# Optimization experiments

Measured on AMD Instinct MI355X. Metric: run time of the kernel, lower is better.

Reference implementation:

```python
import jax, jax.numpy as jnp
import numpy as np

B, L, E, H = 1024, 50, 256, 256
NEG = -1e9          # stands in for -inf masked_fill (exp(NEG) == 0 in fp32)
C_EXPL = 10.0       # tanh_exploration for the pointer head
N_GLIMPSES = 1


def setup_inputs() -> dict:
    key = jax.random.key(0)
    ks = jax.random.split(key, 20)
    s = 1.0 / np.sqrt(H).astype(np.float32)
    return {
        "decoder_input": jax.random.normal(ks[0], (B, E), jnp.float32),
        "embedded_inputs": jax.random.normal(ks[1], (L, B, E), jnp.float32),
        "h0": jax.random.normal(ks[2], (B, H), jnp.float32),
        "c0": jax.random.normal(ks[3], (B, H), jnp.float32),
        "context": jax.random.normal(ks[4], (L, B, H), jnp.float32),
        "init_mask": jnp.zeros((B, L), dtype=bool),
        "lstm_Wih": jax.random.normal(ks[5], (4 * H, E), jnp.float32) * s,
        "lstm_Whh": jax.random.normal(ks[6], (4 * H, H), jnp.float32) * s,
        "lstm_bih": jax.random.normal(ks[7], (4 * H,), jnp.float32) * s,
        "lstm_bhh": jax.random.normal(ks[8], (4 * H,), jnp.float32) * s,
        "gl_Wq": jax.random.normal(ks[9], (H, H), jnp.float32) * s,
        "gl_bq": jax.random.normal(ks[10], (H,), jnp.float32) * s,
        "gl_Wref": jax.random.normal(ks[11], (H, H), jnp.float32) * s,
        "gl_bref": jax.random.normal(ks[12], (H,), jnp.float32) * s,
        "gl_v": jax.random.uniform(ks[13], (H,), jnp.float32, -s, s),
        "pt_Wq": jax.random.normal(ks[14], (H, H), jnp.float32) * s,
        "pt_bq": jax.random.normal(ks[15], (H, H // H * H,)[:1] and (H,), jnp.float32) * s,
        "pt_Wref": jax.random.normal(ks[16], (H, H), jnp.float32) * s,
        "pt_bref": jax.random.normal(ks[17], (H,), jnp.float32) * s,
        "pt_v": jax.random.uniform(ks[18], (H,), jnp.float32, -s, s),
    }


def _attention(Wq, bq, Wref, bref, v, query, context, use_tanh):
    # context: [L,B,H], query: [B,H]
    e = jnp.einsum('lbh,oh->lbo', context, Wref) + bref      # conv1d(k=1) proj of ref
    q = query @ Wq.T + bq                                    # [B,H]
    u = jnp.einsum('lbh,h->bl', jnp.tanh(q[None, :, :] + e), v)
    if use_tanh:
        u = C_EXPL * jnp.tanh(u)
    return e, u


def _lstm_cell(x, h, c, Wih, Whh, bih, bhh):
    g = x @ Wih.T + bih + h @ Whh.T + bhh
    i, f, gg, o = jnp.split(g, 4, axis=1)   # torch LSTMCell gate order: i,f,g,o
    c2 = jax.nn.sigmoid(f) * c + jax.nn.sigmoid(i) * jnp.tanh(gg)
    h2 = jax.nn.sigmoid(o) * jnp.tanh(c2)
    return h2, c2


def reference(decoder_input, embedded_inputs, h0, c0, context, init_mask,
              lstm_Wih, lstm_Whh, lstm_bih, lstm_bhh,
              gl_Wq, gl_bq, gl_Wref, gl_bref, gl_v,
              pt_Wq, pt_bq, pt_Wref, pt_bref, pt_v):
    batch_idx = jnp.arange(B)

    def step(carry, t):
        h, c, mask, idxs, dec_in = carry
        # update_mask(mask, selected), skipped at step 0 (prev_idxs is None)
        safe = jnp.maximum(idxs, 0)
        m2 = mask.at[batch_idx, safe].set(True)
        m2 = m2.at[:, -1].set(jnp.where(m2.all(axis=1), False, m2[:, -1]))
        logit_mask = jnp.where(t == 0, mask, m2)
        # LSTM cell
        hy, cy = _lstm_cell(dec_in, h, c, lstm_Wih, lstm_Whh, lstm_bih, lstm_bhh)
        g_l = hy
        # glimpse attention(s) (mask_glimpses=True)
        for _ in range(N_GLIMPSES):
            e, gl = _attention(gl_Wq, gl_bq, gl_Wref, gl_bref, gl_v, g_l, context, False)
            gl = jnp.where(logit_mask, NEG, gl)
            g_l = jnp.einsum('lbh,bl->bh', e, jax.nn.softmax(gl, axis=1))
        # pointer attention (mask_logits=True)
        _, logits = _attention(pt_Wq, pt_bq, pt_Wref, pt_bref, pt_v, g_l, context, True)
        logits = jnp.where(logit_mask, NEG, logits)
        log_p = jax.nn.log_softmax(logits, axis=1)          # [B,L]
        new_idxs = jax.lax.stop_gradient(jnp.argmax(log_p, axis=1))  # greedy decode (detached)
        new_dec_in = embedded_inputs[new_idxs, batch_idx]   # gather next input [B,E]
        return (hy, cy, logit_mask, new_idxs, new_dec_in), (log_p, new_idxs)

    init = (h0, c0, init_mask, jnp.full((B,), -1, dtype=jnp.int32), decoder_input)
    _, (log_ps, sels) = jax.lax.scan(step, init, jnp.arange(L))
    # stack along time dim 1, as torch.stack(outputs, 1)
    return jnp.transpose(log_ps, (1, 0, 2)), jnp.transpose(sels, (1, 0))
```

## Files before the change

kernel.cpp:

```cpp
#include <hip/hip_runtime.h>
#include <math.h>

#define Bsz 1024
#define Lsz 50
#define Esz 256
#define Hsz 256
#define NEGV (-1e9f)

__device__ __forceinline__ void gl_lds16(const float* g, float* l) {
#if __has_builtin(__builtin_amdgcn_global_load_lds)
    __builtin_amdgcn_global_load_lds(
        (const __attribute__((address_space(1))) unsigned int*)g,
        (__attribute__((address_space(3))) unsigned int*)l, 16, 0, 0);
#else
    *(float4*)l = *(const float4*)g;
#endif
}

__global__ __launch_bounds__(256) void eproj_pack(
    const float* __restrict__ A,
    const float* __restrict__ Wgl, const float* __restrict__ bgl, float* __restrict__ Egl,
    const float* __restrict__ Wpt, const float* __restrict__ bpt, float* __restrict__ Ept,
    const float* __restrict__ WqGl, const float* __restrict__ WqPt,
    float* __restrict__ WqGlP, float* __restrict__ WqPtP)
{
    __shared__ __align__(16) float As[16][68];
    __shared__ __align__(16) float Bs[16][68];
    const int tid = threadIdx.x;

    if (blockIdx.x >= 6400) {
        const int p = blockIdx.x - 6400;
        const int sel = p >> 8;
        const int k = p & 255;
        const float* src = sel ? WqPt : WqGl;
        float*       dst = sel ? WqPtP : WqGlP;
        dst[((size_t)(k >> 2) * 256 + tid) * 4 + (k & 3)] = src[(size_t)tid * 256 + k];
        return;
    }

    const int tx = tid & 15, ty = tid >> 4;
    const int ml = tid >> 2;
    const int kb = (tid & 3) << 2;

    const int x = blockIdx.x;
    const int xcd = x & 7;
    const int j = x >> 3;
    const int mt = xcd * 100 + (j >> 3);
    const int sel = (j >> 2) & 1;
    const int nt = j & 3;
    const float* W    = sel ? Wpt : Wgl;
    const float* bias = sel ? bpt : bgl;
    float*       Eo   = sel ? Ept : Egl;
    const int m0 = mt * 64, n0 = nt * 64;

    float4 a4 = *(const float4*)(A + (size_t)(m0 + ml) * 256 + kb);
    float4 b4 = *(const float4*)(W + (size_t)(n0 + ml) * 256 + kb);

    float acc[4][4] = {};
    for (int k0 = 0; k0 < 256; k0 += 16) {
        As[kb+0][ml] = a4.x; As[kb+1][ml] = a4.y; As[kb+2][ml] = a4.z; As[kb+3][ml] = a4.w;
        Bs[kb+0][ml] = b4.x; Bs[kb+1][ml] = b4.y; Bs[kb+2][ml] = b4.z; Bs[kb+3][ml] = b4.w;
        __syncthreads();
        int k1 = k0 + 16;
        if (k1 < 256) {
            a4 = *(const float4*)(A + (size_t)(m0 + ml) * 256 + k1 + kb);
            b4 = *(const float4*)(W + (size_t)(n0 + ml) * 256 + k1 + kb);
        }
#pragma unroll
        for (int kk = 0; kk < 16; kk++) {
            float4 av = *(const float4*)(&As[kk][ty << 2]);
            float4 bv = *(const float4*)(&Bs[kk][tx << 2]);
            float a_[4] = {av.x, av.y, av.z, av.w};
            float b_[4] = {bv.x, bv.y, bv.z, bv.w};
#pragma unroll
            for (int i = 0; i < 4; i++)
#pragma unroll
                for (int j2 = 0; j2 < 4; j2++) acc[i][j2] = fmaf(a_[i], b_[j2], acc[i][j2]);
        }
        __syncthreads();
    }
#pragma unroll
    for (int i = 0; i < 4; i++) {
        int m = m0 + (ty << 2) + i;
        int bb = m & (Bsz - 1);
        int ll = m >> 10;
#pragma unroll
        for (int j2 = 0; j2 < 4; j2++) {
            int n = n0 + (tx << 2) + j2;
            Eo[(size_t)bb * Lsz * Hsz + (size_t)ll * Hsz + n] = acc[i][j2] + bias[n];
        }
    }
}

__global__ __launch_bounds__(256) void lstm_fused(
    const float* __restrict__ dec, const float* __restrict__ hprev,
    const float* __restrict__ cin,
    const float* __restrict__ Wih, const float* __restrict__ Whh,
    const float* __restrict__ bih, const float* __restrict__ bhh,
    float* __restrict__ hout, float* __restrict__ cout)
{
    __shared__ __align__(16) float As[16][36];
    __shared__ __align__(16) float Bs[16][68];
    const int tid = threadIdx.x;
    const int tx = tid & 15, ty = tid >> 4;
    const int mlA = tid >> 3;
    const int kbA = (tid & 7) << 1;
    const int mlB = tid >> 2;
    const int kbB = (tid & 3) << 2;
    const int m0 = blockIdx.x * 32;
    const int hh0 = blockIdx.y * 16;
    const int wrow = ((mlB >> 4) << 8) + hh0 + (mlB & 15);
    const int pcol = ((mlB & 15) << 2) + (mlB >> 4);

    float2 a2 = *(const float2*)(dec + (size_t)(m0 + mlA) * 256 + kbA);
    float4 b4 = *(const float4*)(Wih + (size_t)wrow * 256 + kbB);

    float acc[2][4] = {};
    for (int k0 = 0; k0 < 512; k0 += 16) {
        As[kbA+0][mlA] = a2.x; As[kbA+1][mlA] = a2.y;
        Bs[kbB+0][pcol] = b4.x; Bs[kbB+1][pcol] = b4.y;
        Bs[kbB+2][pcol] = b4.z; Bs[kbB+3][pcol] = b4.w;
        __syncthreads();
        int k1 = k0 + 16;
        if (k1 < 512) {
            const float* Ap = (k1 < 256) ? dec : hprev;
            const float* Wp = (k1 < 256) ? Wih : Whh;
            int kk0 = k1 & 255;
            a2 = *(const float2*)(Ap + (size_t)(m0 + mlA) * 256 + kk0 + kbA);
            b4 = *(const float4*)(Wp + (size_t)wrow * 256 + kk0 + kbB);
        }
#pragma unroll
        for (int kk = 0; kk < 16; kk++) {
            float2 av = *(const float2*)(&As[kk][ty << 1]);
            float4 bv = *(const float4*)(&Bs[kk][tx << 2]);
            acc[0][0] = fmaf(av.x, bv.x, acc[0][0]);
            acc[0][1] = fmaf(av.x, bv.y, acc[0][1]);
            acc[0][2] = fmaf(av.x, bv.z, acc[0][2]);
            acc[0][3] = fmaf(av.x, bv.w, acc[0][3]);
            acc[1][0] = fmaf(av.y, bv.x, acc[1][0]);
            acc[1][1] = fmaf(av.y, bv.y, acc[1][1]);
            acc[1][2] = fmaf(av.y, bv.z, acc[1][2]);
            acc[1][3] = fmaf(av.y, bv.w, acc[1][3]);
        }
        __syncthreads();
    }

    const int hh = hh0 + tx;
    const float bi0 = bih[hh]       + bhh[hh];
    const float bf  = bih[256 + hh] + bhh[256 + hh];
    const float bg  = bih[512 + hh] + bhh[512 + hh];
    const float bo  = bih[768 + hh] + bhh[768 + hh];
#pragma unroll
    for (int i = 0; i < 2; i++) {
        int m = m0 + (ty << 1) + i;
        float gi = acc[i][0] + bi0;
        float gf = acc[i][1] + bf;
        float gc = acc[i][2] + bg;
        float go = acc[i][3] + bo;
        float ii = 1.0f / (1.0f + expf(-gi));
        float ff = 1.0f / (1.0f + expf(-gf));
        float oo = 1.0f / (1.0f + expf(-go));
        float c2 = ff * cin[(size_t)m * 256 + hh] + ii * tanhf(gc);
        hout[(size_t)m * 256 + hh] = oo * tanhf(c2);
        cout[(size_t)m * 256 + hh] = c2;
    }
}

__global__ __launch_bounds__(256) void attn_row(
    const float* __restrict__ h,
    const float* __restrict__ WqGlP, const float* __restrict__ glbq,
    const float* __restrict__ e_gl, const float* __restrict__ glv,
    const float* __restrict__ WqPtP, const float* __restrict__ ptbq,
    const float* __restrict__ e_pt, const float* __restrict__ ptv,
    int* __restrict__ mask, float* __restrict__ out, int t,
    float* __restrict__ dec, const float* __restrict__ emb)
{
    __shared__ __align__(16) float e_ls[32][256];
    __shared__ __align__(16) float h_s[256];
    __shared__ __align__(16) float q_s[256];
    __shared__ __align__(16) float g_s[256];
    __shared__ float u_s[64];
    __shared__ float p_s[64];
    __shared__ int sel_s;

    const int tid = threadIdx.x;
    const int lane = tid & 63, wave = tid >> 6;
    const int b = blockIdx.x;

    h_s[tid] = h[(size_t)b * 256 + tid];
    __syncthreads();

    {
        float q = glbq[tid];
        const float4* Wp = (const float4*)WqGlP;
#pragma unroll 8
        for (int k4 = 0; k4 < 64; k4++) {
            float4 w  = Wp[(size_t)k4 * 256 + tid];
            float4 hv = ((const float4*)h_s)[k4];
            q = fmaf(hv.x, w.x, q);
            q = fmaf(hv.y, w.y, q);
            q = fmaf(hv.z, w.z, q);
            q = fmaf(hv.w, w.w, q);
        }
        q_s[tid] = q;
    }
    __syncthreads();

    const float* ebg = e_gl + (size_t)b * Lsz * 256;
    const float* ebp = e_pt + (size_t)b * Lsz * 256;
    {
        const float4 q4 = ((const float4*)q_s)[lane];
        const float4 v4 = ((const float4*)glv)[lane];
#pragma unroll
        for (int lp = 0; lp < 13; lp++) {
            const int l = lp * 4 + wave;
            if (lp < 8)
                gl_lds16(ebp + (size_t)l * 256 + (lane << 2), &e_ls[l][0]);
            float x = 0.0f;
            if (l < Lsz) {
                float4 e4 = *(const float4*)(ebg + (size_t)l * 256 + (lane << 2));
                x  = v4.x * tanhf(q4.x + e4.x);
                x += v4.y * tanhf(q4.y + e4.y);
                x += v4.z * tanhf(q4.z + e4.z);
                x += v4.w * tanhf(q4.w + e4.w);
            }
#pragma unroll
            for (int o = 32; o > 0; o >>= 1) x += __shfl_xor(x, o, 64);
            if (lane == 0 && l < Lsz) u_s[l] = x;
        }
    }
    __syncthreads();

    if (wave == 0) {
        const int l = lane;
        const int ml = (l < Lsz && t > 0) ? mask[b * Lsz + l] : 0;
        float logit = (l < Lsz) ? (ml ? NEGV : u_s[l]) : -1e30f;
        float m = logit;
#pragma unroll
        for (int o = 32; o > 0; o >>= 1) m = fmaxf(m, __shfl_xor(m, o, 64));
        float ex = (l < Lsz) ? expf(logit - m) : 0.0f;
        float den = ex;
#pragma unroll
        for (int o = 32; o > 0; o >>= 1) den += __shfl_xor(den, o, 64);
        if (l < Lsz) p_s[l] = ex / den;
    }
    __syncthreads();

    {
        float acc = 0.0f;
        const float* ebh = ebg + tid;
#pragma unroll
        for (int l = 0; l < Lsz; l++)
            acc = fmaf(p_s[l], ebh[(size_t)l * 256], acc);
        g_s[tid] = acc;
    }
    __syncthreads();

    {
        float p = ptbq[tid];
        const float4* Wp = (const float4*)WqPtP;
#pragma unroll 8
        for (int k4 = 0; k4 < 64; k4++) {
            float4 w  = Wp[(size_t)k4 * 256 + tid];
            float4 gv = ((const float4*)g_s)[k4];
            p = fmaf(gv.x, w.x, p);
            p = fmaf(gv.y, w.y, p);
            p = fmaf(gv.z, w.z, p);
            p = fmaf(gv.w, w.w, p);
        }
        q_s[tid] = p;
    }
    __syncthreads();

    {
        const float4 q4 = ((const float4*)q_s)[lane];
        const float4 v4 = ((const float4*)ptv)[lane];
#pragma unroll
        for (int lp = 0; lp < 13; lp++) {
            const int l = lp * 4 + wave;
            float x = 0.0f;
            if (l < Lsz) {
                float4 e4;
                if (lp < 8) e4 = *(const float4*)(&e_ls[l][lane << 2]);
                else        e4 = *(const float4*)(ebp + (size_t)l * 256 + (lane << 2));
                x  = v4.x * tanhf(q4.x + e4.x);
                x += v4.y * tanhf(q4.y + e4.y);
                x += v4.z * tanhf(q4.z + e4.z);
                x += v4.w * tanhf(q4.w + e4.w);
            }
#pragma unroll
            for (int o = 32; o > 0; o >>= 1) x += __shfl_xor(x, o, 64);
            if (lane == 0 && l < Lsz) u_s[l] = x;
        }
    }
    __syncthreads();

    if (wave == 0) {
        const int l = lane;
        const int ml = (l < Lsz && t > 0) ? mask[b * Lsz + l] : 0;
        float logit;
        if (l < Lsz) {
            float u = u_s[l];
            logit = 10.0f * tanhf(u);
            if (ml) logit = NEGV;
        } else logit = -1e30f;

        float m = logit;
#pragma unroll
        for (int o = 32; o > 0; o >>= 1) m = fmaxf(m, __shfl_xor(m, o, 64));
        float ex = (l < Lsz) ? expf(logit - m) : 0.0f;
        float den = ex;
#pragma unroll
        for (int o = 32; o > 0; o >>= 1) den += __shfl_xor(den, o, 64);

        float av = logit; int ai = (l < Lsz) ? l : 63;
#pragma unroll
        for (int o = 32; o > 0; o >>= 1) {
            float ov = __shfl_xor(av, o, 64);
            int   oi = __shfl_xor(ai, o, 64);
            if (ov > av || (ov == av && oi < ai)) { av = ov; ai = oi; }
        }
        const float lse = m + logf(den);
        if (l < Lsz)
            out[(size_t)b * Lsz * Lsz + (size_t)t * Lsz + l] = logit - lse;
        if (l == 0) {
            out[(size_t)Bsz * Lsz * Lsz + (size_t)b * Lsz + t] = (float)ai;
            sel_s = ai;
        }
        int newm = ml | (l == ai);
        unsigned long long bal = __ballot(l >= Lsz ? 1 : newm);
        int all = (bal == 0xFFFFFFFFFFFFFFFFull);
        if (l < Lsz) mask[b * Lsz + l] = (all && l == Lsz - 1) ? 0 : newm;
    }
    __syncthreads();

    {
        const int s = sel_s;
        dec[(size_t)b * 256 + tid] = emb[(size_t)s * Bsz * 256 + (size_t)b * 256 + tid];
    }
}

extern "C" void kernel_launch(void* const* d_in, const int* in_sizes, int n_in,
                              void* d_out, int out_size, void* d_ws, size_t ws_size,
                              hipStream_t stream) {
    const float* decoder_input = (const float*)d_in[0];
    const float* emb           = (const float*)d_in[1];
    const float* h0            = (const float*)d_in[2];
    const float* c0            = (const float*)d_in[3];
    const float* context       = (const float*)d_in[4];
    const float* Wih    = (const float*)d_in[6];
    const float* Whh    = (const float*)d_in[7];
    const float* bih    = (const float*)d_in[8];
    const float* bhh    = (const float*)d_in[9];
    const float* glWq   = (const float*)d_in[10];
    const float* glbq   = (const float*)d_in[11];
    const float* glWref = (const float*)d_in[12];
    const float* glbref = (const float*)d_in[13];
    const float* glv    = (const float*)d_in[14];
    const float* ptWq   = (const float*)d_in[15];
    const float* ptbq   = (const float*)d_in[16];
    const float* ptWref = (const float*)d_in[17];
    const float* ptbref = (const float*)d_in[18];
    const float* ptv    = (const float*)d_in[19];

    float* out = (float*)d_out;

    float* ws    = (float*)d_ws;
    float* e_gl  = ws;
    float* e_pt  = e_gl + (size_t)Bsz * Lsz * Hsz;
    float* WqGlP = e_pt + (size_t)Bsz * Lsz * Hsz;
    float* WqPtP = WqGlP + (size_t)Hsz * Hsz;
    float* hb0   = WqPtP + (size_t)Hsz * Hsz;
    float* hb1   = hb0 + (size_t)Bsz * Hsz;
    float* cb0   = hb1 + (size_t)Bsz * Hsz;
    float* cb1   = cb0 + (size_t)Bsz * Hsz;
    float* dec   = cb1 + (size_t)Bsz * Hsz;
    int*   mask  = (int*)(dec + (size_t)Bsz * Esz);

    float* hbuf[2] = {hb0, hb1};
    float* cbuf[2] = {cb0, cb1};

    eproj_pack<<<dim3(6912), dim3(256), 0, stream>>>(
        context, glWref, glbref, e_gl, ptWref, ptbref, e_pt,
        glWq, ptWq, WqGlP, WqPtP);

    for (int t = 0; t < Lsz; t++) {
        const float* Ain = (t == 0) ? decoder_input : dec;
        const float* hin = (t == 0) ? h0 : hbuf[(t + 1) & 1];
        const float* cin = (t == 0) ? c0 : cbuf[(t + 1) & 1];
        float* hout = hbuf[t & 1];
        float* cout = cbuf[t & 1];

        lstm_fused<<<dim3(32, 16), dim3(256), 0, stream>>>(
            Ain, hin, cin, Wih, Whh, bih, bhh, hout, cout);

        attn_row<<<dim3(1024), dim3(256), 0, stream>>>(
            hout, WqGlP, glbq, e_gl, glv, WqPtP, ptbq, e_pt, ptv,
            mask, out, t, dec, emb);
    }
}
```

Baseline: 4.075 ms.

## Use 512-thread attention blocks with extra waves prefetching context rows into LDS

The attention kernel block size doubles to 512 threads. While the first 256 threads compute the query projections, the extra four waves asynchronously load the first 32 rows of the glimpse (and later the pointer) projected context into LDS. The tanh-score loops are spread over eight waves, and the glimpse weighted sum reads its first 32 rows from LDS. This overlaps the global loads with the matvec and adds parallelism to the score loops. In exchange it raises register pressure under the 512-thread launch bound and leaves half the threads idle during the matvec phases.

```diff
diff --git a/kernel.cpp b/kernel.cpp
--- a/kernel.cpp
+++ b/kernel.cpp
@@ -166,7 +166,7 @@
     }
 }
 
-__global__ __launch_bounds__(256) void attn_row(
+__global__ __launch_bounds__(512, 8) void attn_row(
     const float* __restrict__ h,
     const float* __restrict__ WqGlP, const float* __restrict__ glbq,
     const float* __restrict__ e_gl, const float* __restrict__ glv,
@@ -187,10 +187,13 @@
     const int lane = tid & 63, wave = tid >> 6;
     const int b = blockIdx.x;
 
-    h_s[tid] = h[(size_t)b * 256 + tid];
-    __syncthreads();
-
-    {
+    const float* ebg = e_gl + (size_t)b * Lsz * 256;
+    const float* ebp = e_pt + (size_t)b * Lsz * 256;
+
+    if (tid < 256) h_s[tid] = h[(size_t)b * 256 + tid];
+    __syncthreads();
+
+    if (tid < 256) {
         float q = glbq[tid];
         const float4* Wp = (const float4*)WqGlP;
 #pragma unroll 8
@@ -203,22 +206,25 @@
             q = fmaf(hv.w, w.w, q);
         }
         q_s[tid] = q;
-    }
-    __syncthreads();
-
-    const float* ebg = e_gl + (size_t)b * Lsz * 256;
-    const float* ebp = e_pt + (size_t)b * Lsz * 256;
+    } else {
+        const int r0 = (wave - 4) * 8;
+#pragma unroll
+        for (int j = 0; j < 8; j++)
+            gl_lds16(ebg + (size_t)(r0 + j) * 256 + (lane << 2), &e_ls[r0 + j][0]);
+    }
+    __syncthreads();
+
     {
         const float4 q4 = ((const float4*)q_s)[lane];
         const float4 v4 = ((const float4*)glv)[lane];
 #pragma unroll
-        for (int lp = 0; lp < 13; lp++) {
-            const int l = lp * 4 + wave;
-            if (lp < 8)
-                gl_lds16(ebp + (size_t)l * 256 + (lane << 2), &e_ls[l][0]);
+        for (int lp = 0; lp < 7; lp++) {
+            const int l = lp * 8 + wave;
             float x = 0.0f;
             if (l < Lsz) {
-                float4 e4 = *(const float4*)(ebg + (size_t)l * 256 + (lane << 2));
+                float4 e4;
+                if (lp < 4) e4 = *(const float4*)(&e_ls[l][lane << 2]);
+                else        e4 = *(const float4*)(ebg + (size_t)l * 256 + (lane << 2));
                 x  = v4.x * tanhf(q4.x + e4.x);
                 x += v4.y * tanhf(q4.y + e4.y);
                 x += v4.z * tanhf(q4.z + e4.z);
@@ -246,17 +252,19 @@
     }
     __syncthreads();
 
-    {
+    if (tid < 256) {
         float acc = 0.0f;
         const float* ebh = ebg + tid;
 #pragma unroll
-        for (int l = 0; l < Lsz; l++)
-            acc = fmaf(p_s[l], ebh[(size_t)l * 256], acc);
+        for (int l = 0; l < Lsz; l++) {
+            float ev = (l < 32) ? e_ls[l][tid] : ebh[(size_t)l * 256];
+            acc = fmaf(p_s[l], ev, acc);
+        }
         g_s[tid] = acc;
     }
     __syncthreads();
 
-    {
+    if (tid < 256) {
         float p = ptbq[tid];
         const float4* Wp = (const float4*)WqPtP;
 #pragma unroll 8
@@ -269,6 +277,11 @@
             p = fmaf(gv.w, w.w, p);
         }
         q_s[tid] = p;
+    } else {
+        const int r0 = (wave - 4) * 8;
+#pragma unroll
+        for (int j = 0; j < 8; j++)
+            gl_lds16(ebp + (size_t)(r0 + j) * 256 + (lane << 2), &e_ls[r0 + j][0]);
     }
     __syncthreads();
 
@@ -276,12 +289,12 @@
         const float4 q4 = ((const float4*)q_s)[lane];
         const float4 v4 = ((const float4*)ptv)[lane];
 #pragma unroll
-        for (int lp = 0; lp < 13; lp++) {
-            const int l = lp * 4 + wave;
+        for (int lp = 0; lp < 7; lp++) {
+            const int l = lp * 8 + wave;
             float x = 0.0f;
             if (l < Lsz) {
                 float4 e4;
-                if (lp < 8) e4 = *(const float4*)(&e_ls[l][lane << 2]);
+                if (lp < 4) e4 = *(const float4*)(&e_ls[l][lane << 2]);
                 else        e4 = *(const float4*)(ebp + (size_t)l * 256 + (lane << 2));
                 x  = v4.x * tanhf(q4.x + e4.x);
                 x += v4.y * tanhf(q4.y + e4.y);
@@ -334,7 +347,7 @@
     }
     __syncthreads();
 
-    {
+    if (tid < 256) {
         const int s = sel_s;
         dec[(size_t)b * 256 + tid] = emb[(size_t)s * Bsz * 256 + (size_t)b * 256 + tid];
     }
@@ -394,7 +407,7 @@
         lstm_fused<<<dim3(32, 16), dim3(256), 0, stream>>>(
             Ain, hin, cin, Wih, Whh, bih, bhh, hout, cout);
 
-        attn_row<<<dim3(1024), dim3(256), 0, stream>>>(
+        attn_row<<<dim3(1024), dim3(512), 0, stream>>>(
             hout, WqGlP, glbq, e_gl, glv, WqPtP, ptbq, e_pt, ptv,
             mask, out, t, dec, emb);
     }
```

Measured after the change: 4.622 ms. 13.4% more time.

## Double-buffer LSTM GEMM tiles and prefetch glimpse context rows into LDS

Applied to the files above, without the earlier changes.

The LSTM gate GEMM moves to a K-tile of 32 with two LDS buffers. The next tile is stored after the compute, so each iteration needs one barrier instead of two. In the attention kernel, the first 32 rows of the glimpse context projection are copied into LDS with async global-to-LDS loads while the query matvec runs. The glimpse score and weighted-sum loops then read those rows from LDS, and the pointer context is prefetched the same way during the pointer query matvec. This roughly doubles LDS use in the LSTM kernel and relies on barriers to order the async LDS loads before they are read.

```diff
diff --git a/kernel.cpp b/kernel.cpp
--- a/kernel.cpp
+++ b/kernel.cpp
@@ -99,12 +99,12 @@
     const float* __restrict__ bih, const float* __restrict__ bhh,
     float* __restrict__ hout, float* __restrict__ cout)
 {
-    __shared__ __align__(16) float As[16][36];
-    __shared__ __align__(16) float Bs[16][68];
+    __shared__ __align__(16) float As[2][32][36];
+    __shared__ __align__(16) float Bs[2][32][68];
     const int tid = threadIdx.x;
     const int tx = tid & 15, ty = tid >> 4;
     const int mlA = tid >> 3;
-    const int kbA = (tid & 7) << 1;
+    const int kbA = (tid & 7) << 2;
     const int mlB = tid >> 2;
     const int kbB = (tid & 3) << 2;
     const int m0 = blockIdx.x * 32;
@@ -112,27 +112,34 @@
     const int wrow = ((mlB >> 4) << 8) + hh0 + (mlB & 15);
     const int pcol = ((mlB & 15) << 2) + (mlB >> 4);
 
-    float2 a2 = *(const float2*)(dec + (size_t)(m0 + mlA) * 256 + kbA);
-    float4 b4 = *(const float4*)(Wih + (size_t)wrow * 256 + kbB);
+    float4 a4  = *(const float4*)(dec + (size_t)(m0 + mlA) * 256 + kbA);
+    float4 b4a = *(const float4*)(Wih + (size_t)wrow * 256 + kbB);
+    float4 b4b = *(const float4*)(Wih + (size_t)wrow * 256 + 16 + kbB);
+
+    As[0][kbA+0][mlA] = a4.x; As[0][kbA+1][mlA] = a4.y;
+    As[0][kbA+2][mlA] = a4.z; As[0][kbA+3][mlA] = a4.w;
+    Bs[0][kbB+0][pcol] = b4a.x; Bs[0][kbB+1][pcol] = b4a.y;
+    Bs[0][kbB+2][pcol] = b4a.z; Bs[0][kbB+3][pcol] = b4a.w;
+    Bs[0][16+kbB+0][pcol] = b4b.x; Bs[0][16+kbB+1][pcol] = b4b.y;
+    Bs[0][16+kbB+2][pcol] = b4b.z; Bs[0][16+kbB+3][pcol] = b4b.w;
+    __syncthreads();
 
     float acc[2][4] = {};
-    for (int k0 = 0; k0 < 512; k0 += 16) {
-        As[kbA+0][mlA] = a2.x; As[kbA+1][mlA] = a2.y;
-        Bs[kbB+0][pcol] = b4.x; Bs[kbB+1][pcol] = b4.y;
-        Bs[kbB+2][pcol] = b4.z; Bs[kbB+3][pcol] = b4.w;
-        __syncthreads();
-        int k1 = k0 + 16;
-        if (k1 < 512) {
+    for (int kt = 0; kt < 16; kt++) {
+        const int cur = kt & 1;
+        if (kt < 15) {
+            const int k1 = (kt + 1) << 5;
             const float* Ap = (k1 < 256) ? dec : hprev;
             const float* Wp = (k1 < 256) ? Wih : Whh;
-            int kk0 = k1 & 255;
-            a2 = *(const float2*)(Ap + (size_t)(m0 + mlA) * 256 + kk0 + kbA);
-            b4 = *(const float4*)(Wp + (size_t)wrow * 256 + kk0 + kbB);
-        }
-#pragma unroll
-        for (int kk = 0; kk < 16; kk++) {
-            float2 av = *(const float2*)(&As[kk][ty << 1]);
-            float4 bv = *(const float4*)(&Bs[kk][tx << 2]);
+            const int kk0 = k1 & 255;
+            a4  = *(const float4*)(Ap + (size_t)(m0 + mlA) * 256 + kk0 + kbA);
+            b4a = *(const float4*)(Wp + (size_t)wrow * 256 + kk0 + kbB);
+            b4b = *(const float4*)(Wp + (size_t)wrow * 256 + kk0 + 16 + kbB);
+        }
+#pragma unroll
+        for (int kk = 0; kk < 32; kk++) {
+            float2 av = *(const float2*)(&As[cur][kk][ty << 1]);
+            float4 bv = *(const float4*)(&Bs[cur][kk][tx << 2]);
             acc[0][0] = fmaf(av.x, bv.x, acc[0][0]);
             acc[0][1] = fmaf(av.x, bv.y, acc[0][1]);
             acc[0][2] = fmaf(av.x, bv.z, acc[0][2]);
@@ -142,7 +149,16 @@
             acc[1][2] = fmaf(av.y, bv.z, acc[1][2]);
             acc[1][3] = fmaf(av.y, bv.w, acc[1][3]);
         }
-        __syncthreads();
+        if (kt < 15) {
+            const int nxt = cur ^ 1;
+            As[nxt][kbA+0][mlA] = a4.x; As[nxt][kbA+1][mlA] = a4.y;
+            As[nxt][kbA+2][mlA] = a4.z; As[nxt][kbA+3][mlA] = a4.w;
+            Bs[nxt][kbB+0][pcol] = b4a.x; Bs[nxt][kbB+1][pcol] = b4a.y;
+            Bs[nxt][kbB+2][pcol] = b4a.z; Bs[nxt][kbB+3][pcol] = b4a.w;
+            Bs[nxt][16+kbB+0][pcol] = b4b.x; Bs[nxt][16+kbB+1][pcol] = b4b.y;
+            Bs[nxt][16+kbB+2][pcol] = b4b.z; Bs[nxt][16+kbB+3][pcol] = b4b.w;
+            __syncthreads();
+        }
     }
 
     const int hh = hh0 + tx;
@@ -187,6 +203,9 @@
     const int lane = tid & 63, wave = tid >> 6;
     const int b = blockIdx.x;
 
+    const float* ebg = e_gl + (size_t)b * Lsz * 256;
+    const float* ebp = e_pt + (size_t)b * Lsz * 256;
+
     h_s[tid] = h[(size_t)b * 256 + tid];
     __syncthreads();
 
@@ -195,6 +214,8 @@
         const float4* Wp = (const float4*)WqGlP;
 #pragma unroll 8
         for (int k4 = 0; k4 < 64; k4++) {
+            if (k4 < 32 && wave == (k4 & 3))
+                gl_lds16(ebg + (size_t)k4 * 256 + (lane << 2), &e_ls[k4][0]);
             float4 w  = Wp[(size_t)k4 * 256 + tid];
             float4 hv = ((const float4*)h_s)[k4];
             q = fmaf(hv.x, w.x, q);
@@ -206,19 +227,17 @@
     }
     __syncthreads();
 
-    const float* ebg = e_gl + (size_t)b * Lsz * 256;
-    const float* ebp = e_pt + (size_t)b * Lsz * 256;
     {
         const float4 q4 = ((const float4*)q_s)[lane];
         const float4 v4 = ((const float4*)glv)[lane];
 #pragma unroll
         for (int lp = 0; lp < 13; lp++) {
             const int l = lp * 4 + wave;
-            if (lp < 8)
-                gl_lds16(ebp + (size_t)l * 256 + (lane << 2), &e_ls[l][0]);
             float x = 0.0f;
             if (l < Lsz) {
-                float4 e4 = *(const float4*)(ebg + (size_t)l * 256 + (lane << 2));
+                float4 e4;
+                if (lp < 8) e4 = *(const float4*)(&e_ls[l][lane << 2]);
+                else        e4 = *(const float4*)(ebg + (size_t)l * 256 + (lane << 2));
                 x  = v4.x * tanhf(q4.x + e4.x);
                 x += v4.y * tanhf(q4.y + e4.y);
                 x += v4.z * tanhf(q4.z + e4.z);
@@ -250,8 +269,10 @@
         float acc = 0.0f;
         const float* ebh = ebg + tid;
 #pragma unroll
-        for (int l = 0; l < Lsz; l++)
-            acc = fmaf(p_s[l], ebh[(size_t)l * 256], acc);
+        for (int l = 0; l < Lsz; l++) {
+            float ev = (l < 32) ? e_ls[l][tid] : ebh[(size_t)l * 256];
+            acc = fmaf(p_s[l], ev, acc);
+        }
         g_s[tid] = acc;
     }
     __syncthreads();
@@ -261,6 +282,8 @@
         const float4* Wp = (const float4*)WqPtP;
 #pragma unroll 8
         for (int k4 = 0; k4 < 64; k4++) {
+            if (k4 < 32 && wave == (k4 & 3))
+                gl_lds16(ebp + (size_t)k4 * 256 + (lane << 2), &e_ls[k4][0]);
             float4 w  = Wp[(size_t)k4 * 256 + tid];
             float4 gv = ((const float4*)g_s)[k4];
             p = fmaf(gv.x, w.x, p);
```

Result: no change. 4.086 ms (+0.3%).
